# Kernel optimization log

Measured on AMD Instinct MI355X. Metric: run time of the kernel, lower is better.

## Reference

```python
import jax, jax.numpy as jnp
import numpy as np

DIM = 1024
HEADS = 16

def setup_inputs() -> dict:
    key = jax.random.key(0)
    ks = jax.random.split(key, 5)
    x = jax.random.normal(ks[0], (4, 2048, DIM), dtype=jnp.float32)
    s = 1.0 / np.sqrt(DIM)
    Wqkv = jax.random.normal(ks[1], (DIM, 3 * DIM), dtype=jnp.float32) * s
    bqkv = jnp.zeros((3 * DIM,), dtype=jnp.float32)
    Wproj = jax.random.normal(ks[2], (DIM, DIM), dtype=jnp.float32) * s
    bproj = jnp.zeros((DIM,), dtype=jnp.float32)
    return {"x": x, "Wqkv": Wqkv, "bqkv": bqkv, "Wproj": Wproj, "bproj": bproj}

def reference(x, Wqkv, bqkv, Wproj, bproj):
    B, N, D = x.shape
    H = HEADS
    hd = D // H
    scale = hd ** (-0.5)
    qkv = x @ Wqkv + bqkv                      # [B, N, 3D]
    q, k, v = jnp.split(qkv, 3, axis=-1)
    # [B, N, H, hd] -> [B, H, N, hd]
    q = q.reshape(B, N, H, hd).transpose(0, 2, 1, 3)
    k = k.reshape(B, N, H, hd).transpose(0, 2, 1, 3)
    v = v.reshape(B, N, H, hd).transpose(0, 2, 1, 3)
    attn = jnp.einsum('bhqd,bhkd->bhqk', q, k) * scale
    attn = jax.nn.softmax(attn, axis=-1)
    out = jnp.einsum('bhqk,bhkd->bhqd', attn, v)
    out = out.transpose(0, 2, 1, 3).reshape(B, N, D)
    return out @ Wproj + bproj
```

## Files before the change

### kernel.cpp

```cpp
#include <hip/hip_runtime.h>
#include <hip/hip_bf16.h>
#include <math.h>


typedef __bf16 bf16;
typedef __bf16 bf16x4 __attribute__((ext_vector_type(4)));
typedef __bf16 bf16x8 __attribute__((ext_vector_type(8)));
typedef float f32x4 __attribute__((ext_vector_type(4)));

#define AS1(p) ((const __attribute__((address_space(1))) void*)(p))
#define AS3(p) ((__attribute__((address_space(3))) void*)(p))

__device__ __forceinline__ void async16(const void* g, void* l) {
    __builtin_amdgcn_global_load_lds(AS1(g), AS3(l), 16, 0, 0);
}

#define QSCALE 0.18033688011112042f


__global__ void cvt_f32_bf16(const float* __restrict__ in, bf16* __restrict__ out, int n4) {
    int i = blockIdx.x * blockDim.x + threadIdx.x;
    if (i < n4) {
        float4 v = ((const float4*)in)[i];
        bf16x4 o;
        o.x = (bf16)v.x; o.y = (bf16)v.y; o.z = (bf16)v.z; o.w = (bf16)v.w;
        ((bf16x4*)out)[i] = o;
    }
}

__global__ void transpose_cvt(const float* __restrict__ in, bf16* __restrict__ out, int K, int N) {
    __shared__ float t[32][33];
    const int n0 = blockIdx.x * 32, k0 = blockIdx.y * 32;
    const int tx = threadIdx.x, ty = threadIdx.y;
    #pragma unroll
    for (int j = 0; j < 32; j += 8)
        t[ty + j][tx] = in[(size_t)(k0 + ty + j) * N + n0 + tx];
    __syncthreads();
    #pragma unroll
    for (int j = 0; j < 32; j += 8)
        out[(size_t)(n0 + ty + j) * K + k0 + tx] = (bf16)t[tx][ty + j];
}


__device__ __forceinline__ void gemm_mainloop(const bf16* __restrict__ A,
                                              const bf16* __restrict__ Bt,
                                              int K, int m0, int n0,
                                              bf16* As, bf16* Bs, f32x4 acc[4][4]) {
    const int tid = threadIdx.x;
    const int wave = tid >> 6, lane = tid & 63;
    const int c = lane & 15, quad = lane >> 4;
    const int wm = (wave & 1) * 64, wn = (wave >> 1) * 64;

    const int ci0 = (wave * 2 + 0) * 64 + lane;
    const int ci1 = (wave * 2 + 1) * 64 + lane;
    const bf16* ga0 = A  + (size_t)(m0 + (ci0 >> 2)) * K + (ci0 & 3) * 8;
    const bf16* ga1 = A  + (size_t)(m0 + (ci1 >> 2)) * K + (ci1 & 3) * 8;
    const bf16* gb0 = Bt + (size_t)(n0 + (ci0 >> 2)) * K + (ci0 & 3) * 8;
    const bf16* gb1 = Bt + (size_t)(n0 + (ci1 >> 2)) * K + (ci1 & 3) * 8;
    bf16* la0 = As + (wave * 2 + 0) * 512;
    bf16* la1 = As + (wave * 2 + 1) * 512;
    bf16* lb0 = Bs + (wave * 2 + 0) * 512;
    bf16* lb1 = Bs + (wave * 2 + 1) * 512;

    for (int kt = 0; kt < K; kt += 32) {
        async16(ga0 + kt, la0);
        async16(ga1 + kt, la1);
        async16(gb0 + kt, lb0);
        async16(gb1 + kt, lb1);
        __syncthreads();
        bf16x8 af[4], bfr[4];
        #pragma unroll
        for (int i = 0; i < 4; i++)
            af[i] = *(const bf16x8*)(As + (wm + i * 16 + c) * 32 + quad * 8);
        #pragma unroll
        for (int j = 0; j < 4; j++)
            bfr[j] = *(const bf16x8*)(Bs + (wn + j * 16 + c) * 32 + quad * 8);
        #pragma unroll
        for (int i = 0; i < 4; i++)
            #pragma unroll
            for (int j = 0; j < 4; j++)
                acc[i][j] = __builtin_amdgcn_mfma_f32_16x16x32_bf16(af[i], bfr[j], acc[i][j], 0, 0, 0);
        __syncthreads();
    }
}


__global__ __launch_bounds__(256) void gemm_qkv(const bf16* __restrict__ A,
                                                const bf16* __restrict__ Bt,
                                                const float* __restrict__ bias,
                                                bf16* __restrict__ Qb,
                                                bf16* __restrict__ Kb,
                                                bf16* __restrict__ Vtb) {
    __shared__ __align__(16) bf16 As[128 * 32];
    __shared__ __align__(16) bf16 Bs[128 * 32];
    f32x4 acc[4][4] = {};
    const int m0 = blockIdx.x * 128, n0 = blockIdx.y * 128;
    gemm_mainloop(A, Bt, 1024, m0, n0, As, Bs, acc);

    const int tid = threadIdx.x;
    const int wave = tid >> 6, lane = tid & 63;
    const int c = lane & 15, quad = lane >> 4;
    const int wm = (wave & 1) * 64, wn = (wave >> 1) * 64;
    const int sel = n0 >> 10;
    bf16* QK = (sel == 0) ? Qb : Kb;
    const float qs = (sel == 0) ? QSCALE : 1.0f;

    #pragma unroll
    for (int j = 0; j < 4; j++) {
        const int nfull = n0 + wn + j * 16 + c;
        const int nmod = nfull & 1023;
        const int h = nmod >> 6, e = nmod & 63;
        const float bv = bias[nfull];
        #pragma unroll
        for (int i = 0; i < 4; i++) {
            const int mbase = m0 + wm + i * 16 + quad * 4;
            const int b = mbase >> 11, t = mbase & 2047;
            if (sel < 2) {
                bf16* dst = QK + (((size_t)(b * 16 + h) * 2048 + t) * 64 + e);
                #pragma unroll
                for (int r = 0; r < 4; r++)
                    dst[(size_t)r * 64] = (bf16)((acc[i][j][r] + bv) * qs);
            } else {
                bf16* dst = Vtb + ((size_t)(b * 16 + h) * 64 + e) * 2048 + t;
                bf16x4 v;
                v.x = (bf16)(acc[i][j][0] + bv);
                v.y = (bf16)(acc[i][j][1] + bv);
                v.z = (bf16)(acc[i][j][2] + bv);
                v.w = (bf16)(acc[i][j][3] + bv);
                *(bf16x4*)dst = v;
            }
        }
    }
}


__global__ __launch_bounds__(256, 3) void attn_kernel(const bf16* __restrict__ Q,
                                                      const bf16* __restrict__ Kg,
                                                      const bf16* __restrict__ Vt,
                                                      bf16* __restrict__ Out) {
    __shared__ __align__(16) bf16 Ks[128 * 64];
    __shared__ __align__(16) bf16 Vs[64 * 128];
    __shared__ __align__(16) bf16 Pl[4 * 2 * 16 * 72];

    const int bh = blockIdx.x, qt = blockIdx.y;
    const int tid = threadIdx.x;
    const int wave = tid >> 6, lane = tid & 63;
    const int c = lane & 15, quad = lane >> 4;

    const bf16* Qb = Q  + (size_t)bh * 2048 * 64;
    const bf16* Kb = Kg + (size_t)bh * 2048 * 64;
    const bf16* Vb = Vt + (size_t)bh * 64 * 2048;
    bf16* pw = Pl + wave * 2304;

    const int qbase = qt * 128 + wave * 32;

    bf16x8 qf[2][2];
    #pragma unroll
    for (int i = 0; i < 2; i++)
        #pragma unroll
        for (int ks = 0; ks < 2; ks++)
            qf[i][ks] = *(const bf16x8*)(Qb + (size_t)(qbase + i * 16 + c) * 64 + ks * 32 + quad * 8);

    f32x4 lsum[2] = {};
    f32x4 o[2][4] = {};

    for (int kv = 0; kv < 16; kv++) {
        const bf16* Kt = Kb + (size_t)kv * 8192;

        #pragma unroll
        for (int t = 0; t < 4; t++) {
            const int s = t * 256 + tid;
            const int row = s >> 3, cl = s & 7;
            const int cg = cl ^ (row & 7);
            async16(Kt + row * 64 + cg * 8, Ks + (size_t)(t * 256 + wave * 64) * 8);
        }
        #pragma unroll
        for (int t = 0; t < 4; t++) {
            const int s = t * 256 + tid;
            const int row = s >> 4, cl = s & 15;
            const int cg = cl ^ (row & 15);
            async16(Vb + (size_t)row * 2048 + kv * 128 + cg * 8,
                    Vs + (size_t)(t * 256 + wave * 64) * 8);
        }
        __syncthreads();

        #pragma unroll
        for (int h = 0; h < 2; h++) {
            #pragma unroll
            for (int j = 0; j < 4; j++) {
                const int rowK = (h * 4 + j) * 16 + c;
                const int sw = c & 7;
                bf16x8 kf0 = *(const bf16x8*)(Ks + ((size_t)rowK * 8 + (quad ^ sw)) * 8);
                bf16x8 kf1 = *(const bf16x8*)(Ks + ((size_t)rowK * 8 + ((4 + quad) ^ sw)) * 8);
                f32x4 s0 = {}, s1 = {};
                s0 = __builtin_amdgcn_mfma_f32_16x16x32_bf16(kf0, qf[0][0], s0, 0, 0, 0);
                s0 = __builtin_amdgcn_mfma_f32_16x16x32_bf16(kf1, qf[0][1], s0, 0, 0, 0);
                s1 = __builtin_amdgcn_mfma_f32_16x16x32_bf16(kf0, qf[1][0], s1, 0, 0, 0);
                s1 = __builtin_amdgcn_mfma_f32_16x16x32_bf16(kf1, qf[1][1], s1, 0, 0, 0);
                #pragma unroll
                for (int r = 0; r < 4; r++) { s0[r] = exp2f(s0[r]); s1[r] = exp2f(s1[r]); }
                lsum[0] += s0;
                lsum[1] += s1;
                bf16x4 p0, p1;
                p0.x = (bf16)s0[0]; p0.y = (bf16)s0[1]; p0.z = (bf16)s0[2]; p0.w = (bf16)s0[3];
                p1.x = (bf16)s1[0]; p1.y = (bf16)s1[1]; p1.z = (bf16)s1[2]; p1.w = (bf16)s1[3];
                *(bf16x4*)(pw + c * 72 + j * 16 + quad * 4) = p0;
                *(bf16x4*)(pw + (16 + c) * 72 + j * 16 + quad * 4) = p1;
            }
            #pragma unroll
            for (int gksl = 0; gksl < 2; gksl++) {
                const int gks = h * 2 + gksl;
                bf16x8 vf[4];
                #pragma unroll
                for (int n2 = 0; n2 < 4; n2++) {
                    const int rowV = n2 * 16 + c;
                    vf[n2] = *(const bf16x8*)(Vs + ((size_t)rowV * 16 + ((gks * 4 + quad) ^ c)) * 8);
                }
                bf16x8 pf0 = *(const bf16x8*)(pw + c * 72 + gksl * 32 + quad * 8);
                bf16x8 pf1 = *(const bf16x8*)(pw + (16 + c) * 72 + gksl * 32 + quad * 8);
                #pragma unroll
                for (int n2 = 0; n2 < 4; n2++) {
                    o[0][n2] = __builtin_amdgcn_mfma_f32_16x16x32_bf16(pf0, vf[n2], o[0][n2], 0, 0, 0);
                    o[1][n2] = __builtin_amdgcn_mfma_f32_16x16x32_bf16(pf1, vf[n2], o[1][n2], 0, 0, 0);
                }
            }
        }
        __syncthreads();
    }

    const int b = bh >> 4, hh = bh & 15;
    #pragma unroll
    for (int i = 0; i < 2; i++) {
        float lh = (lsum[i][0] + lsum[i][1]) + (lsum[i][2] + lsum[i][3]);
        lh += __shfl_xor(lh, 16);
        lh += __shfl_xor(lh, 32);
        const float li0 = __shfl(lh, quad * 4 + 0);
        const float li1 = __shfl(lh, quad * 4 + 1);
        const float li2 = __shfl(lh, quad * 4 + 2);
        const float li3 = __shfl(lh, quad * 4 + 3);
        const float inv[4] = {1.f / li0, 1.f / li1, 1.f / li2, 1.f / li3};
        #pragma unroll
        for (int r = 0; r < 4; r++) {
            const int token = b * 2048 + qbase + i * 16 + quad * 4 + r;
            #pragma unroll
            for (int n2 = 0; n2 < 4; n2++) {
                const int feat = hh * 64 + n2 * 16 + c;
                Out[(size_t)token * 1024 + feat] = (bf16)(o[i][n2][r] * inv[r]);
            }
        }
    }
}


__global__ __launch_bounds__(256) void gemm_proj(const bf16* __restrict__ A,
                                                 const bf16* __restrict__ Bt,
                                                 const float* __restrict__ bias,
                                                 float* __restrict__ Out) {
    __shared__ __align__(16) bf16 As[128 * 32];
    __shared__ __align__(16) bf16 Bs[128 * 32];
    f32x4 acc[4][4] = {};
    const int m0 = blockIdx.x * 128, n0 = blockIdx.y * 128;
    gemm_mainloop(A, Bt, 1024, m0, n0, As, Bs, acc);

    const int tid = threadIdx.x;
    const int wave = tid >> 6, lane = tid & 63;
    const int c = lane & 15, quad = lane >> 4;
    const int wm = (wave & 1) * 64, wn = (wave >> 1) * 64;

    #pragma unroll
    for (int j = 0; j < 4; j++) {
        const int nn = n0 + wn + j * 16 + c;
        const float bv = bias[nn];
        #pragma unroll
        for (int i = 0; i < 4; i++) {
            const int m = m0 + wm + i * 16 + quad * 4;
            #pragma unroll
            for (int r = 0; r < 4; r++)
                Out[(size_t)(m + r) * 1024 + nn] = acc[i][j][r] + bv;
        }
    }
}


extern "C" void kernel_launch(void* const* d_in, const int* in_sizes, int n_in,
                              void* d_out, int out_size, void* d_ws, size_t ws_size,
                              hipStream_t stream) {
    const float* x     = (const float*)d_in[0];
    const float* Wqkv  = (const float*)d_in[1];
    const float* bqkv  = (const float*)d_in[2];
    const float* Wproj = (const float*)d_in[3];
    const float* bproj = (const float*)d_in[4];
    float* out = (float*)d_out;

    char* ws = (char*)d_ws;
    bf16* xb     = (bf16*)(ws);
    bf16* wqkvt  = (bf16*)(ws + 16777216);
    bf16* wprojt = (bf16*)(ws + 23068672);
    bf16* Qb     = (bf16*)(ws + 25165824);
    bf16* Kb     = (bf16*)(ws + 41943040);
    bf16* Vtb    = (bf16*)(ws + 58720256);
    bf16* attno  = xb;

    cvt_f32_bf16<<<8192, 256, 0, stream>>>(x, xb, 2097152);
    transpose_cvt<<<dim3(96, 32), dim3(32, 8), 0, stream>>>(Wqkv, wqkvt, 1024, 3072);
    transpose_cvt<<<dim3(32, 32), dim3(32, 8), 0, stream>>>(Wproj, wprojt, 1024, 1024);
    gemm_qkv<<<dim3(64, 24), 256, 0, stream>>>(xb, wqkvt, bqkv, Qb, Kb, Vtb);
    attn_kernel<<<dim3(64, 16), 256, 0, stream>>>(Qb, Kb, Vtb, attno);
    gemm_proj<<<dim3(64, 8), 256, 0, stream>>>(attno, wprojt, bproj, out);
}
```

Measured before the change: 300.0 us.

## Double-buffer K/V tiles in attention kernel with 64-key stages

Splits the 128-key K/V tile into two 64-key LDS buffers and issues the async load of the next stage before computing the current one, so global-to-LDS transfers overlap the MFMA and exp work. It also precomputes the swizzled LDS pointers, uses the raw hardware exp2 builtin, and raises wave priority around MFMA groups. The cost is more pointer registers and a sync after every 64-key stage, which may affect the three-blocks-per-CU occupancy target.

```diff
diff --git a/kernel.cpp b/kernel.cpp
--- a/kernel.cpp
+++ b/kernel.cpp
@@ -14,6 +14,12 @@
 __device__ __forceinline__ void async16(const void* g, void* l) {
     __builtin_amdgcn_global_load_lds(AS1(g), AS3(l), 16, 0, 0);
 }
+
+#if __has_builtin(__builtin_amdgcn_exp2f)
+#define EXP2(x) __builtin_amdgcn_exp2f(x)
+#else
+#define EXP2(x) exp2f(x)
+#endif
 
 #define QSCALE 0.18033688011112042f
 
@@ -134,12 +140,61 @@
 }
 
 
+#define ATTN_STAGE(B) do { \
+    async16(kS0, kD0_##B); async16(kS1, kD1_##B); \
+    async16(vS0, vD0_##B); async16(vS1, vD1_##B); \
+    kS0 += 4096; kS1 += 4096; vS0 += 64; vS1 += 64; \
+} while (0)
+
+#define ATTN_COMPUTE(B) do { \
+    _Pragma("unroll") \
+    for (int j = 0; j < 4; j++) { \
+        bf16x8 kf0 = *(const bf16x8*)(kb0_##B + j * 1024); \
+        bf16x8 kf1 = *(const bf16x8*)(kb1_##B + j * 1024); \
+        f32x4 s0 = {}, s1 = {}; \
+        __builtin_amdgcn_s_setprio(1); \
+        s0 = __builtin_amdgcn_mfma_f32_16x16x32_bf16(kf0, qf[0][0], s0, 0, 0, 0); \
+        s0 = __builtin_amdgcn_mfma_f32_16x16x32_bf16(kf1, qf[0][1], s0, 0, 0, 0); \
+        s1 = __builtin_amdgcn_mfma_f32_16x16x32_bf16(kf0, qf[1][0], s1, 0, 0, 0); \
+        s1 = __builtin_amdgcn_mfma_f32_16x16x32_bf16(kf1, qf[1][1], s1, 0, 0, 0); \
+        __builtin_amdgcn_s_setprio(0); \
+        _Pragma("unroll") \
+        for (int r = 0; r < 4; r++) { s0[r] = EXP2(s0[r]); s1[r] = EXP2(s1[r]); } \
+        lsum[0] += s0; \
+        lsum[1] += s1; \
+        bf16x4 p0, p1; \
+        p0.x = (bf16)s0[0]; p0.y = (bf16)s0[1]; p0.z = (bf16)s0[2]; p0.w = (bf16)s0[3]; \
+        p1.x = (bf16)s1[0]; p1.y = (bf16)s1[1]; p1.z = (bf16)s1[2]; p1.w = (bf16)s1[3]; \
+        *(bf16x4*)(pwa + j * 16) = p0; \
+        *(bf16x4*)(pwb + j * 16) = p1; \
+    } \
+    _Pragma("unroll") \
+    for (int gks = 0; gks < 2; gks++) { \
+        const bf16* vbg = gks ? vb1_##B : vb0_##B; \
+        bf16x8 vf[4]; \
+        _Pragma("unroll") \
+        for (int n2 = 0; n2 < 4; n2++) \
+            vf[n2] = *(const bf16x8*)(vbg + n2 * 1024); \
+        bf16x8 pf0 = *(const bf16x8*)(pra + gks * 32); \
+        bf16x8 pf1 = *(const bf16x8*)(prb + gks * 32); \
+        __builtin_amdgcn_s_setprio(1); \
+        _Pragma("unroll") \
+        for (int n2 = 0; n2 < 4; n2++) { \
+            o[0][n2] = __builtin_amdgcn_mfma_f32_16x16x32_bf16(pf0, vf[n2], o[0][n2], 0, 0, 0); \
+            o[1][n2] = __builtin_amdgcn_mfma_f32_16x16x32_bf16(pf1, vf[n2], o[1][n2], 0, 0, 0); \
+        } \
+        __builtin_amdgcn_s_setprio(0); \
+    } \
+} while (0)
+
 __global__ __launch_bounds__(256, 3) void attn_kernel(const bf16* __restrict__ Q,
                                                       const bf16* __restrict__ Kg,
                                                       const bf16* __restrict__ Vt,
                                                       bf16* __restrict__ Out) {
-    __shared__ __align__(16) bf16 Ks[128 * 64];
-    __shared__ __align__(16) bf16 Vs[64 * 128];
+    __shared__ __align__(16) bf16 Ks0[64 * 64];
+    __shared__ __align__(16) bf16 Ks1[64 * 64];
+    __shared__ __align__(16) bf16 Vs0[64 * 64];
+    __shared__ __align__(16) bf16 Vs1[64 * 64];
     __shared__ __align__(16) bf16 Pl[4 * 2 * 16 * 72];
 
     const int bh = blockIdx.x, qt = blockIdx.y;
@@ -147,9 +202,7 @@
     const int wave = tid >> 6, lane = tid & 63;
     const int c = lane & 15, quad = lane >> 4;
 
-    const bf16* Qb = Q  + (size_t)bh * 2048 * 64;
-    const bf16* Kb = Kg + (size_t)bh * 2048 * 64;
-    const bf16* Vb = Vt + (size_t)bh * 64 * 2048;
+    const bf16* Qb = Q + (size_t)bh * 2048 * 64;
     bf16* pw = Pl + wave * 2304;
 
     const int qbase = qt * 128 + wave * 32;
@@ -161,70 +214,48 @@
         for (int ks = 0; ks < 2; ks++)
             qf[i][ks] = *(const bf16x8*)(Qb + (size_t)(qbase + i * 16 + c) * 64 + ks * 32 + quad * 8);
 
+    const int s0i = tid, s1i = 256 + tid;
+    const int rk0 = s0i >> 3, cg0 = (s0i & 7) ^ (rk0 & 7);
+    const int rk1 = s1i >> 3, cg1 = (s1i & 7) ^ (rk1 & 7);
+    const bf16* kS0 = Kg + (size_t)bh * 2048 * 64 + rk0 * 64 + cg0 * 8;
+    const bf16* kS1 = Kg + (size_t)bh * 2048 * 64 + rk1 * 64 + cg1 * 8;
+    const bf16* vS0 = Vt + (size_t)bh * 64 * 2048 + (size_t)rk0 * 2048 + cg0 * 8;
+    const bf16* vS1 = Vt + (size_t)bh * 64 * 2048 + (size_t)rk1 * 2048 + cg1 * 8;
+    bf16* kD0_0 = Ks0 + (size_t)(wave * 64) * 8;
+    bf16* kD1_0 = Ks0 + (size_t)(256 + wave * 64) * 8;
+    bf16* kD0_1 = Ks1 + (size_t)(wave * 64) * 8;
+    bf16* kD1_1 = Ks1 + (size_t)(256 + wave * 64) * 8;
+    bf16* vD0_0 = Vs0 + (size_t)(wave * 64) * 8;
+    bf16* vD1_0 = Vs0 + (size_t)(256 + wave * 64) * 8;
+    bf16* vD0_1 = Vs1 + (size_t)(wave * 64) * 8;
+    bf16* vD1_1 = Vs1 + (size_t)(256 + wave * 64) * 8;
+
+    const int sw = c & 7;
+    const int ch0 = (quad ^ sw) * 8, ch1 = ((quad ^ sw) ^ 4) * 8;
+    const bf16* kb0_0 = Ks0 + c * 64 + ch0;
+    const bf16* kb1_0 = Ks0 + c * 64 + ch1;
+    const bf16* kb0_1 = Ks1 + c * 64 + ch0;
+    const bf16* kb1_1 = Ks1 + c * 64 + ch1;
+    const bf16* vb0_0 = Vs0 + c * 64 + ch0;
+    const bf16* vb1_0 = Vs0 + c * 64 + ch1;
+    const bf16* vb0_1 = Vs1 + c * 64 + ch0;
+    const bf16* vb1_1 = Vs1 + c * 64 + ch1;
+    bf16* pwa = pw + c * 72 + quad * 4;
+    bf16* pwb = pwa + 16 * 72;
+    const bf16* pra = pw + c * 72 + quad * 8;
+    const bf16* prb = pra + 16 * 72;
+
     f32x4 lsum[2] = {};
     f32x4 o[2][4] = {};
 
-    for (int kv = 0; kv < 16; kv++) {
-        const bf16* Kt = Kb + (size_t)kv * 8192;
-
-        #pragma unroll
-        for (int t = 0; t < 4; t++) {
-            const int s = t * 256 + tid;
-            const int row = s >> 3, cl = s & 7;
-            const int cg = cl ^ (row & 7);
-            async16(Kt + row * 64 + cg * 8, Ks + (size_t)(t * 256 + wave * 64) * 8);
-        }
-        #pragma unroll
-        for (int t = 0; t < 4; t++) {
-            const int s = t * 256 + tid;
-            const int row = s >> 4, cl = s & 15;
-            const int cg = cl ^ (row & 15);
-            async16(Vb + (size_t)row * 2048 + kv * 128 + cg * 8,
-                    Vs + (size_t)(t * 256 + wave * 64) * 8);
-        }
+    ATTN_STAGE(0);
+    __syncthreads();
+    for (int kv2 = 0; kv2 < 16; kv2++) {
+        ATTN_STAGE(1);
+        ATTN_COMPUTE(0);
         __syncthreads();
-
-        #pragma unroll
-        for (int h = 0; h < 2; h++) {
-            #pragma unroll
-            for (int j = 0; j < 4; j++) {
-                const int rowK = (h * 4 + j) * 16 + c;
-                const int sw = c & 7;
-                bf16x8 kf0 = *(const bf16x8*)(Ks + ((size_t)rowK * 8 + (quad ^ sw)) * 8);
-                bf16x8 kf1 = *(const bf16x8*)(Ks + ((size_t)rowK * 8 + ((4 + quad) ^ sw)) * 8);
-                f32x4 s0 = {}, s1 = {};
-                s0 = __builtin_amdgcn_mfma_f32_16x16x32_bf16(kf0, qf[0][0], s0, 0, 0, 0);
-                s0 = __builtin_amdgcn_mfma_f32_16x16x32_bf16(kf1, qf[0][1], s0, 0, 0, 0);
-                s1 = __builtin_amdgcn_mfma_f32_16x16x32_bf16(kf0, qf[1][0], s1, 0, 0, 0);
-                s1 = __builtin_amdgcn_mfma_f32_16x16x32_bf16(kf1, qf[1][1], s1, 0, 0, 0);
-                #pragma unroll
-                for (int r = 0; r < 4; r++) { s0[r] = exp2f(s0[r]); s1[r] = exp2f(s1[r]); }
-                lsum[0] += s0;
-                lsum[1] += s1;
-                bf16x4 p0, p1;
-                p0.x = (bf16)s0[0]; p0.y = (bf16)s0[1]; p0.z = (bf16)s0[2]; p0.w = (bf16)s0[3];
-                p1.x = (bf16)s1[0]; p1.y = (bf16)s1[1]; p1.z = (bf16)s1[2]; p1.w = (bf16)s1[3];
-                *(bf16x4*)(pw + c * 72 + j * 16 + quad * 4) = p0;
-                *(bf16x4*)(pw + (16 + c) * 72 + j * 16 + quad * 4) = p1;
-            }
-            #pragma unroll
-            for (int gksl = 0; gksl < 2; gksl++) {
-                const int gks = h * 2 + gksl;
-                bf16x8 vf[4];
-                #pragma unroll
-                for (int n2 = 0; n2 < 4; n2++) {
-                    const int rowV = n2 * 16 + c;
-                    vf[n2] = *(const bf16x8*)(Vs + ((size_t)rowV * 16 + ((gks * 4 + quad) ^ c)) * 8);
-                }
-                bf16x8 pf0 = *(const bf16x8*)(pw + c * 72 + gksl * 32 + quad * 8);
-                bf16x8 pf1 = *(const bf16x8*)(pw + (16 + c) * 72 + gksl * 32 + quad * 8);
-                #pragma unroll
-                for (int n2 = 0; n2 < 4; n2++) {
-                    o[0][n2] = __builtin_amdgcn_mfma_f32_16x16x32_bf16(pf0, vf[n2], o[0][n2], 0, 0, 0);
-                    o[1][n2] = __builtin_amdgcn_mfma_f32_16x16x32_bf16(pf1, vf[n2], o[1][n2], 0, 0, 0);
-                }
-            }
-        }
+        if (kv2 < 15) ATTN_STAGE(0);
+        ATTN_COMPUTE(1);
         __syncthreads();
     }
 
```

Result: faster. 272.2 us (-9.3%).
